# Performance work log

Measured on AMD Instinct MI355X. Metric: run time of the kernel, lower is better.

## Reference

```python
import jax, jax.numpy as jnp
import numpy as np

N, E, G = 50000, 800000, 512
C = 128          # in_channels = hidden_out_channel = out_channel
K = 3            # Chebyshev order (nb_filters)
NUM_EMB = 119    # largest OGB atom feature cardinality (padded common table)
EPS = 1e-5


def setup_inputs() -> dict:
    key = jax.random.key(0)
    ks = jax.random.split(key, 12)
    s = 0.05
    return {
        "atom_emb": jax.random.normal(ks[0], (9, NUM_EMB, C), jnp.float32) * s,
        "W1": jax.random.normal(ks[1], (K, C, C), jnp.float32) * s,
        "b1": jnp.zeros((C,), jnp.float32),
        "W3": jax.random.normal(ks[2], (K, C, C), jnp.float32) * s,
        "b3": jnp.zeros((C,), jnp.float32),
        "gamma": jnp.ones((C,), jnp.float32),
        "beta": jnp.zeros((C,), jnp.float32),
        "lw1": jax.random.normal(ks[3], (C, 16), jnp.float32) * s,
        "lb1": jnp.zeros((16,), jnp.float32),
        "lw2": jax.random.normal(ks[4], (16, 2), jnp.float32) * s,
        "lb2": jnp.zeros((2,), jnp.float32),
        "x": jax.random.randint(ks[5], (N, 9), 0, 2),
        "edge_index": jax.random.randint(ks[6], (2, E), 0, N),
        "batch": jnp.sort(jax.random.randint(ks[7], (N,), 0, G)),
    }


def _cheb_conv(h, row, col, norm, W, b):
    # PyG ChebConv, sym norm, lambda_max=2 => Lhat = -D^{-1/2} A D^{-1/2} (zero diag)
    def Lhat(z):
        return jax.ops.segment_sum(norm[:, None] * z[col], row, num_segments=N)
    Tx1 = Lhat(h)                      # T_1 = Lhat x
    Tx2 = 2.0 * Lhat(Tx1) - h          # T_2 = 2 Lhat T_1 - T_0
    return h @ W[0] + Tx1 @ W[1] + Tx2 @ W[2] + b


def reference(atom_emb, W1, b1, W3, b3, gamma, beta, lw1, lb1, lw2, lb2,
              x, edge_index, batch):
    row, col = edge_index[0], edge_index[1]
    # symmetric normalization weights (deg computed on row, as in get_laplacian)
    deg = jax.ops.segment_sum(jnp.ones((E,), jnp.float32), row, num_segments=N)
    dis = jnp.where(deg > 0, jax.lax.rsqrt(jnp.maximum(deg, 1.0)), 0.0)
    norm = -(dis[row] * dis[col])      # [E]

    # AtomEncoder: sum of 9 per-feature embeddings -> [N, C]
    h = atom_emb[jnp.arange(9), x].sum(axis=1)

    h = jax.nn.relu(_cheb_conv(h, row, col, norm, W1, b1))   # conv1
    h = jax.nn.relu(_cheb_conv(h, row, col, norm, W3, b3))   # conv3 (conv2 unused)

    # BatchNorm over nodes (training-mode batch stats, biased var)
    mu = h.mean(axis=0)
    var = jnp.mean((h - mu) ** 2, axis=0)
    h = (h - mu) * jax.lax.rsqrt(var + EPS) * gamma + beta

    # global_mean_pool over graphs
    sums = jax.ops.segment_sum(h, batch, num_segments=G)
    cnt = jax.ops.segment_sum(jnp.ones((N,), jnp.float32), batch, num_segments=G)
    pooled = sums / jnp.maximum(cnt, 1.0)[:, None]           # [G, C]

    out = jax.nn.relu(pooled @ lw1 + lb1) @ lw2 + lb2        # [G, 2]
    return out
```

## Files before the change

### kernel.cpp

```cpp
#include <hip/hip_runtime.h>
#include <hip/hip_bf16.h>

typedef __hip_bfloat16 bf16;
#define BN_EPS 1e-5f

typedef __attribute__((ext_vector_type(8))) short bf16x8;
typedef __attribute__((ext_vector_type(4))) float f32x4;

__device__ __forceinline__ float b2f(bf16 v){ return __bfloat162float(v); }
__device__ __forceinline__ float bu2f(unsigned short u){
  union { unsigned int i; float f; } x; x.i = ((unsigned int)u) << 16; return x.f;
}
__device__ __forceinline__ unsigned short f2bu(float f){
  bf16 b = __float2bfloat16(f);
  union { bf16 b; unsigned short u; } x; x.b = b; return x.u;
}
__device__ __forceinline__ float ldw(const void* p, size_t i, int wf){
  return wf ? ((const float*)p)[i] : b2f(((const bf16*)p)[i]);
}
__device__ __forceinline__ void up2(unsigned int w, float& lo, float& hi){
  union { unsigned int i; float f; } L, H;
  L.i = w << 16; H.i = w & 0xffff0000u;
  lo = L.f; hi = H.f;
}

__global__ void k_zero(int* __restrict__ p, int n,
                       const unsigned int* __restrict__ gbits, int* __restrict__ flag){
  int i = blockIdx.x * blockDim.x + threadIdx.x;
  if (i == 0) *flag = (gbits[0] == 0x3F800000u) ? 1 : 0;
  if (i < n) p[i] = 0;
}

__global__ __launch_bounds__(256) void k_bhist(const int* __restrict__ row, int E,
                                               int* __restrict__ gcnt){
  __shared__ int hist[256];
  int t = threadIdx.x;
  hist[t] = 0;
  __syncthreads();
  int base = blockIdx.x * 4096;
  #pragma unroll
  for (int j = 0; j < 16; ++j){
    int e = base + (j << 8) + t;
    if (e < E) atomicAdd(&hist[row[e] >> 8], 1);
  }
  __syncthreads();
  int h = hist[t];
  if (h > 0) atomicAdd(&gcnt[t], h);
}

__global__ __launch_bounds__(256) void k_bbase(const int* __restrict__ gcnt,
    int* __restrict__ bucketBase, int* __restrict__ gcur, int* __restrict__ rp, int N){
  __shared__ int ss[256];
  int t = threadIdx.x;
  int v = gcnt[t];
  ss[t] = v; __syncthreads();
  for (int o = 1; o < 256; o <<= 1){
    int u = (t >= o) ? ss[t - o] : 0;
    __syncthreads();
    ss[t] += u;
    __syncthreads();
  }
  int ex = ss[t] - v;
  bucketBase[t] = ex;
  gcur[t] = ex;
  if (t == 255){ bucketBase[256] = ss[255]; rp[N] = ss[255]; }
}

__global__ __launch_bounds__(256) void k_prep(int N,
    const void* __restrict__ Wa, unsigned short* __restrict__ WTa,
    const void* __restrict__ Wb, unsigned short* __restrict__ WTb,
    const void* __restrict__ emb, const int* __restrict__ x, int NE,
    unsigned short* __restrict__ h, const int* __restrict__ flag){
  int b = blockIdx.x;
  int t = threadIdx.x;
  int wf = *flag;
  if (b < 384){
    int id = b * 256 + t;
    const void* W = (id < 49152) ? Wa : Wb;
    unsigned short* WT = (id < 49152) ? WTa : WTb;
    int i = (id < 49152) ? id : id - 49152;
    int r = i >> 7, n = i & 127;
    WT[(size_t)n * 384 + r] = f2bu(ldw(W, (size_t)r * 128 + n, wf));
    return;
  }
  int gid = (b - 384) * 256 + t;
  int n = gid >> 4, c8 = (gid & 15) << 3;
  if (n >= N) return;
  float s[8];
  #pragma unroll
  for (int j = 0; j < 8; ++j) s[j] = 0.f;
  #pragma unroll
  for (int f = 0; f < 9; ++f){
    int idx = x[n * 9 + f];
    size_t base = ((size_t)(f * NE + idx) << 7) + c8;
    if (wf){
      const float* ep = (const float*)emb + base;
      #pragma unroll
      for (int j = 0; j < 8; ++j) s[j] += ep[j];
    } else {
      uint4 v = *(const uint4*)((const unsigned short*)emb + base);
      float lo, hi;
      up2(v.x, lo, hi); s[0] += lo; s[1] += hi;
      up2(v.y, lo, hi); s[2] += lo; s[3] += hi;
      up2(v.z, lo, hi); s[4] += lo; s[5] += hi;
      up2(v.w, lo, hi); s[6] += lo; s[7] += hi;
    }
  }
  uint4 r;
  r.x = ((unsigned int)f2bu(s[1]) << 16) | f2bu(s[0]);
  r.y = ((unsigned int)f2bu(s[3]) << 16) | f2bu(s[2]);
  r.z = ((unsigned int)f2bu(s[5]) << 16) | f2bu(s[4]);
  r.w = ((unsigned int)f2bu(s[7]) << 16) | f2bu(s[6]);
  *(uint4*)(h + ((size_t)n << 7) + c8) = r;
}

__global__ __launch_bounds__(256) void k_bfill1(const int* __restrict__ row,
    const int* __restrict__ col, int E,
    int* __restrict__ gcur, unsigned int* __restrict__ ebuf){
  __shared__ int hist[256];
  __shared__ int curs[256];
  int t = threadIdx.x;
  hist[t] = 0;
  __syncthreads();
  int base = blockIdx.x * 4096;
  int r[16], c[16];
  #pragma unroll
  for (int j = 0; j < 16; ++j){
    int e = base + (j << 8) + t;
    if (e < E){
      r[j] = row[e]; c[j] = col[e];
      atomicAdd(&hist[r[j] >> 8], 1);
    } else r[j] = -1;
  }
  __syncthreads();
  int h = hist[t];
  if (h > 0) curs[t] = atomicAdd(&gcur[t], h);
  __syncthreads();
  #pragma unroll
  for (int j = 0; j < 16; ++j){
    if (r[j] >= 0){
      int p = atomicAdd(&curs[r[j] >> 8], 1);
      ebuf[p] = ((unsigned int)c[j] << 8) | ((unsigned int)r[j] & 255u);
    }
  }
}

__global__ __launch_bounds__(256) void k_bfill2a(const unsigned int* __restrict__ ebuf,
    const int* __restrict__ bucketBase, int N,
    int* __restrict__ rp, float* __restrict__ dis){
  __shared__ int cnt[256];
  __shared__ int ss[256];
  int b = blockIdx.x, t = threadIdx.x;
  cnt[t] = 0;
  __syncthreads();
  int beg = bucketBase[b], end = bucketBase[b + 1];
  for (int p = beg + t; p < end; p += 256)
    atomicAdd(&cnt[ebuf[p] & 255u], 1);
  __syncthreads();
  int v = cnt[t];
  ss[t] = v; __syncthreads();
  for (int o = 1; o < 256; o <<= 1){
    int u = (t >= o) ? ss[t - o] : 0;
    __syncthreads();
    ss[t] += u;
    __syncthreads();
  }
  int idx = (b << 8) + t;
  if (idx < N){
    rp[idx] = beg + ss[t] - v;
    dis[idx] = (v > 0) ? rsqrtf((float)v) : 0.f;
  }
}

__global__ __launch_bounds__(256) void k_bfill2b(const unsigned int* __restrict__ ebuf,
    const int* __restrict__ bucketBase, const int* __restrict__ rp, int N,
    const float* __restrict__ dis, int2* __restrict__ cpack){
  __shared__ int lcur[256];
  __shared__ float sdis[256];
  int b = blockIdx.x, t = threadIdx.x;
  int idx = (b << 8) + t;
  lcur[t] = (idx < N) ? rp[idx] : 0;
  sdis[t] = (idx < N) ? dis[idx] : 0.f;
  __syncthreads();
  int beg = bucketBase[b], end = bucketBase[b + 1];
  for (int p = beg + t; p < end; p += 256){
    unsigned int pw = ebuf[p];
    int c = (int)(pw >> 8);
    int rl = (int)(pw & 255u);
    float nm = -(sdis[rl] * dis[c]);
    int slot = atomicAdd(&lcur[rl], 1);
    cpack[slot] = make_int2(c, __float_as_int(nm));
  }
}

__global__ __launch_bounds__(256) void k_spmm(const unsigned short* __restrict__ in,
    const int* __restrict__ rp, const int2* __restrict__ cpack,
    float alpha, const unsigned short* __restrict__ other, float beta,
    unsigned short* __restrict__ out, int N){
  int w = (blockIdx.x * 256 + threadIdx.x) >> 6;
  int lane = threadIdx.x & 63;
  if (w >= N) return;
  int half = lane >> 5, hl = lane & 31;
  int p0 = rp[w], p1 = rp[w + 1];
  float a0 = 0.f, a1 = 0.f, a2 = 0.f, a3 = 0.f;
  for (int p = p0; p < p1; p += 64){
    int m = p1 - p; if (m > 64) m = 64;
    int cj = 0; float nj = 0.f;
    if (lane < m){
      int2 pk = cpack[p + lane];
      cj = pk.x; nj = __int_as_float(pk.y);
    }
    for (int j = 0; j < m; j += 4){
      int e0 = j + half, e1 = j + 2 + half;
      int c0 = (e0 < m) ? __shfl(cj, e0) : -1;
      float w0 = __shfl(nj, e0);
      int c1 = (e1 < m) ? __shfl(cj, e1) : -1;
      float w1 = __shfl(nj, e1);
      if (c0 >= 0){
        ushort4 v = *(const ushort4*)(in + (((size_t)c0) << 7) + (hl << 2));
        a0 += w0 * bu2f(v.x); a1 += w0 * bu2f(v.y);
        a2 += w0 * bu2f(v.z); a3 += w0 * bu2f(v.w);
      }
      if (c1 >= 0){
        ushort4 v = *(const ushort4*)(in + (((size_t)c1) << 7) + (hl << 2));
        a0 += w1 * bu2f(v.x); a1 += w1 * bu2f(v.y);
        a2 += w1 * bu2f(v.z); a3 += w1 * bu2f(v.w);
      }
    }
  }
  a0 += __shfl_xor(a0, 32);
  a1 += __shfl_xor(a1, 32);
  a2 += __shfl_xor(a2, 32);
  a3 += __shfl_xor(a3, 32);
  if (half == 0){
    size_t o = (((size_t)w) << 7) + (hl << 2);
    a0 *= alpha; a1 *= alpha; a2 *= alpha; a3 *= alpha;
    if (other){
      ushort4 ov = *(const ushort4*)(other + o);
      a0 += beta * bu2f(ov.x); a1 += beta * bu2f(ov.y);
      a2 += beta * bu2f(ov.z); a3 += beta * bu2f(ov.w);
    }
    ushort4 r;
    r.x = f2bu(a0); r.y = f2bu(a1); r.z = f2bu(a2); r.w = f2bu(a3);
    *(ushort4*)(out + o) = r;
  }
}

__global__ __launch_bounds__(256) void k_conv(const unsigned short* __restrict__ X,
    const unsigned short* __restrict__ T1, const unsigned short* __restrict__ T2,
    const unsigned short* __restrict__ WT,
    const void* __restrict__ bias,
    unsigned short* __restrict__ Y, int N, const int* __restrict__ flag,
    float* __restrict__ bns){
  int wf = *flag;
  __shared__ unsigned short As[128 * 40];
  __shared__ unsigned short Ws[128 * 40];
  int t = threadIdx.x;
  int wv = t >> 6, lane = t & 63;
  int m16 = lane & 15, quad = lane >> 4;
  int n0 = blockIdx.x * 128;

  f32x4 acc[2][8];
  #pragma unroll
  for (int i = 0; i < 2; ++i)
    #pragma unroll
    for (int j = 0; j < 8; ++j) acc[i][j] = (f32x4){0.f, 0.f, 0.f, 0.f};

  for (int kc = 0; kc < 12; ++kc){
    const unsigned short* src = (kc < 4) ? X : ((kc < 8) ? T1 : T2);
    int koff = (kc & 3) << 5;
    int kg = kc << 5;
    #pragma unroll
    for (int i = 0; i < 2; ++i){
      int id = t + (i << 8);
      int r = id >> 2, ks = id & 3;
      int node = n0 + r;
      uint4 v = make_uint4(0, 0, 0, 0);
      if (node < N) v = *(const uint4*)(src + ((size_t)node << 7) + koff + (ks << 3));
      *(uint4*)((void*)(As + r * 40 + (ks << 3))) = v;
    }
    #pragma unroll
    for (int i = 0; i < 2; ++i){
      int id = t + (i << 8);
      int n = id >> 2, ks = id & 3;
      uint4 v = *(const uint4*)(WT + (size_t)n * 384 + kg + (ks << 3));
      *(uint4*)((void*)(Ws + n * 40 + (ks << 3))) = v;
    }
    __syncthreads();
    bf16x8 af[2];
    af[0] = *(const bf16x8*)((const void*)(As + (32 * wv + m16) * 40 + (quad << 3)));
    af[1] = *(const bf16x8*)((const void*)(As + (32 * wv + 16 + m16) * 40 + (quad << 3)));
    #pragma unroll
    for (int tn = 0; tn < 8; ++tn){
      bf16x8 bf_ = *(const bf16x8*)((const void*)(Ws + (16 * tn + m16) * 40 + (quad << 3)));
      acc[0][tn] = __builtin_amdgcn_mfma_f32_16x16x32_bf16(af[0], bf_, acc[0][tn], 0, 0, 0);
      acc[1][tn] = __builtin_amdgcn_mfma_f32_16x16x32_bf16(af[1], bf_, acc[1][tn], 0, 0, 0);
    }
    __syncthreads();
  }
  float bv[8];
  #pragma unroll
  for (int tn = 0; tn < 8; ++tn) bv[tn] = ldw(bias, 16 * tn + m16, wf);
  float ps[8], pq[8];
  #pragma unroll
  for (int tn = 0; tn < 8; ++tn){ ps[tn] = 0.f; pq[tn] = 0.f; }
  #pragma unroll
  for (int ri = 0; ri < 2; ++ri){
    #pragma unroll
    for (int r = 0; r < 4; ++r){
      int node = n0 + 32 * wv + 16 * ri + quad * 4 + r;
      if (node < N){
        #pragma unroll
        for (int tn = 0; tn < 8; ++tn){
          float v = fmaxf(acc[ri][tn][r] + bv[tn], 0.f);
          Y[((size_t)node << 7) + 16 * tn + m16] = f2bu(v);
          ps[tn] += v; pq[tn] += v * v;
        }
      }
    }
  }
  if (bns){
    float* redf = (float*)As;
    int rg = (wv << 2) | quad;
    #pragma unroll
    for (int tn = 0; tn < 8; ++tn) redf[rg * 128 + tn * 16 + m16] = ps[tn];
    __syncthreads();
    if (t < 128){
      float a = 0.f;
      #pragma unroll
      for (int r = 0; r < 16; ++r) a += redf[r * 128 + t];
      atomicAdd(&bns[t], a);
    }
    __syncthreads();
    #pragma unroll
    for (int tn = 0; tn < 8; ++tn) redf[rg * 128 + tn * 16 + m16] = pq[tn];
    __syncthreads();
    if (t < 128){
      float a = 0.f;
      #pragma unroll
      for (int r = 0; r < 16; ++r) a += redf[r * 128 + t];
      atomicAdd(&bns[128 + t], a);
    }
  }
}

__device__ __forceinline__ int lbound(const int* a, int n, int key){
  int lo = 0, hi = n;
  while (lo < hi){ int mid = (lo + hi) >> 1; if (a[mid] < key) lo = mid + 1; else hi = mid; }
  return lo;
}

__global__ __launch_bounds__(128) void k_pool(const unsigned short* __restrict__ h,
    const int* __restrict__ batchv, int N, const float* __restrict__ bns,
    const void* __restrict__ gamma, const void* __restrict__ beta,
    const void* __restrict__ lw1, const void* __restrict__ lb1,
    const void* __restrict__ lw2, const void* __restrict__ lb2,
    void* __restrict__ out, const int* __restrict__ flag){
  int wf = *flag;
  int g = blockIdx.x;
  int t = threadIdx.x;
  int c8 = (t & 15) << 3;
  int rg = t >> 4;
  __shared__ int slo, shi;
  if (t == 0){ slo = lbound(batchv, N, g); shi = lbound(batchv, N, g + 1); }
  __syncthreads();
  int lo = slo, hi = shi, cnt = hi - lo;
  float s[8];
  #pragma unroll
  for (int j = 0; j < 8; ++j) s[j] = 0.f;
  for (int n = lo + rg; n < hi; n += 8){
    uint4 v = *(const uint4*)(h + ((size_t)n << 7) + c8);
    float a, b;
    up2(v.x, a, b); s[0] += a; s[1] += b;
    up2(v.y, a, b); s[2] += a; s[3] += b;
    up2(v.z, a, b); s[4] += a; s[5] += b;
    up2(v.w, a, b); s[6] += a; s[7] += b;
  }
  __shared__ float red[8][128];
  *(float4*)(&red[rg][c8])     = (float4){s[0], s[1], s[2], s[3]};
  *(float4*)(&red[rg][c8 + 4]) = (float4){s[4], s[5], s[6], s[7]};
  __syncthreads();
  int c = t;
  float acc = 0.f;
  #pragma unroll
  for (int r = 0; r < 8; ++r) acc += red[r][c];
  float pooled = acc / (float)(cnt > 0 ? cnt : 1);
  float mu = bns[c] / (float)N;
  float var = bns[128 + c] / (float)N - mu * mu;
  float sc = ldw(gamma, c, wf) * rsqrtf(var + BN_EPS);
  float sh = ldw(beta, c, wf) - mu * sc;
  float pb = (cnt > 0) ? (pooled * sc + sh) : 0.f;
  __shared__ float sp[128];
  __shared__ float hid[16];
  sp[c] = pb; __syncthreads();
  if (c < 16){
    float sm = ldw(lb1, c, wf);
    for (int i = 0; i < 128; ++i) sm += sp[i] * ldw(lw1, i * 16 + c, wf);
    hid[c] = fmaxf(sm, 0.f);
  }
  __syncthreads();
  if (c < 2){
    float sm = ldw(lb2, c, wf);
    for (int j = 0; j < 16; ++j) sm += hid[j] * ldw(lw2, j * 2 + c, wf);
    if (wf) ((float*)out)[g * 2 + c] = sm;
    else    ((bf16*)out)[g * 2 + c] = __float2bfloat16(sm);
  }
}

extern "C" void kernel_launch(void* const* d_in, const int* in_sizes, int n_in,
                              void* d_out, int out_size, void* d_ws, size_t ws_size,
                              hipStream_t stream){
  const void* emb   = d_in[0];
  const void* W1    = d_in[1];
  const void* b1    = d_in[2];
  const void* W3    = d_in[3];
  const void* b3    = d_in[4];
  const void* gamma = d_in[5];
  const void* beta  = d_in[6];
  const void* lw1   = d_in[7];
  const void* lb1   = d_in[8];
  const void* lw2   = d_in[9];
  const void* lb2   = d_in[10];
  const int* x      = (const int*)d_in[11];
  const int* ei     = (const int*)d_in[12];
  const int* batchv = (const int*)d_in[13];
  (void)n_in; (void)ws_size;

  int N  = in_sizes[13];
  int E  = in_sizes[12] / 2;
  int NE = in_sizes[0] / (9 * 128);
  int G  = out_size / 2;
  const int* row = ei;
  const int* col = ei + E;

  char* ws = (char*)d_ws;
  size_t off = 0;
  auto alloc = [&](size_t bytes) -> char* {
    char* p = ws + off;
    off += (bytes + 255) & ~(size_t)255;
    return p;
  };
  int*   flag = (int*)alloc(4);
  int*   gcnt = (int*)alloc(256 * 4);
  float* bns  = (float*)alloc(256 * 4);
  int*   bucketBase = (int*)alloc(257 * 4);
  int*   gcur = (int*)alloc(256 * 4);
  int*   rp   = (int*)alloc((size_t)(N + 1) * 4);
  float* dis  = (float*)alloc((size_t)N * 4);
  unsigned int* ebuf = (unsigned int*)alloc((size_t)E * 4);
  int2*  cpack = (int2*)alloc((size_t)E * 8);
  unsigned short* wt1 = (unsigned short*)alloc(49152 * 2);
  unsigned short* wt2 = (unsigned short*)alloc(49152 * 2);
  size_t fb = ((size_t)N * 128 * 2 + 255) & ~(size_t)255;
  unsigned short* Hf = (unsigned short*)alloc(fb);
  unsigned short* Tf = (unsigned short*)alloc(fb);
  unsigned short* Zf = (unsigned short*)alloc(fb);

  k_zero<<<2, 256, 0, stream>>>(gcnt, 512, (const unsigned int*)gamma, flag);

  int ebk = (E + 4095) / 4096;
  int NB  = (N + 255) / 256;
  k_bhist<<<ebk, 256, 0, stream>>>(row, E, gcnt);
  k_bbase<<<1, 256, 0, stream>>>(gcnt, bucketBase, gcur, rp, N);
  int pb = 384 + (int)(((size_t)N * 16 + 255) / 256);
  k_prep<<<pb, 256, 0, stream>>>(N, W1, wt1, W3, wt2, emb, x, NE, Hf, flag);
  k_bfill1<<<ebk, 256, 0, stream>>>(row, col, E, gcur, ebuf);
  k_bfill2a<<<NB, 256, 0, stream>>>(ebuf, bucketBase, N, rp, dis);
  k_bfill2b<<<NB, 256, 0, stream>>>(ebuf, bucketBase, rp, N, dis, cpack);

  int sb = (N + 3) / 4;
  int cb = (N + 127) / 128;
  k_spmm<<<sb, 256, 0, stream>>>(Hf, rp, cpack, 1.f, nullptr, 0.f, Tf, N);
  k_spmm<<<sb, 256, 0, stream>>>(Tf, rp, cpack, 2.f, Hf, -1.f, Zf, N);
  k_conv<<<cb, 256, 0, stream>>>(Hf, Tf, Zf, wt1, b1, Hf, N, flag, nullptr);
  k_spmm<<<sb, 256, 0, stream>>>(Hf, rp, cpack, 1.f, nullptr, 0.f, Tf, N);
  k_spmm<<<sb, 256, 0, stream>>>(Tf, rp, cpack, 2.f, Hf, -1.f, Zf, N);
  k_conv<<<cb, 256, 0, stream>>>(Hf, Tf, Zf, wt2, b3, Hf, N, flag, bns);

  k_pool<<<G, 128, 0, stream>>>(Hf, batchv, N, bns, gamma, beta, lw1, lb1, lw2, lb2,
                                d_out, flag);
}
```

Before: 352.6 us.

## Fold Chebyshev T2 recurrence into weights and widen SpMM gather to 16-byte loads

Uses the identity T2 = 2·L·T1 − X to fold the recurrence into the weight matrices at prep time: W0' = W0 − W2 and W2' = 2·W2. The SpMM kernel then writes the raw L·T1 result without the axpy epilogue. The SpMM is also restructured so that four quarter-waves each process different edges with 8-channel uint4 loads, then reduce across quarters with shuffles. This removes the extra read of the 'other' tensor and the cross-lane broadcast of edge data. The cost is a slight change to bf16 rounding behaviour.

```diff
diff --git a/kernel.cpp b/kernel.cpp
--- a/kernel.cpp
+++ b/kernel.cpp
@@ -80,7 +80,12 @@
     unsigned short* WT = (id < 49152) ? WTa : WTb;
     int i = (id < 49152) ? id : id - 49152;
     int r = i >> 7, n = i & 127;
-    WT[(size_t)n * 384 + r] = f2bu(ldw(W, (size_t)r * 128 + n, wf));
+    float v;
+    if (r < 128)       v = ldw(W, (size_t)r * 128 + n, wf)
+                         - ldw(W, ((size_t)(256 + r)) * 128 + n, wf);
+    else if (r < 256)  v = ldw(W, (size_t)r * 128 + n, wf);
+    else               v = 2.f * ldw(W, (size_t)r * 128 + n, wf);
+    WT[(size_t)n * 384 + r] = f2bu(v);
     return;
   }
   int gid = (b - 384) * 256 + t;
@@ -195,54 +200,58 @@
 
 __global__ __launch_bounds__(256) void k_spmm(const unsigned short* __restrict__ in,
     const int* __restrict__ rp, const int2* __restrict__ cpack,
-    float alpha, const unsigned short* __restrict__ other, float beta,
     unsigned short* __restrict__ out, int N){
   int w = (blockIdx.x * 256 + threadIdx.x) >> 6;
+  if (w >= N) return;
   int lane = threadIdx.x & 63;
-  if (w >= N) return;
-  int half = lane >> 5, hl = lane & 31;
-  int p0 = rp[w], p1 = rp[w + 1];
+  int quad = lane >> 4, ql = lane & 15;
+  int p1 = rp[w + 1];
+  int p = rp[w] + quad;
+  const unsigned short* inq = in + (ql << 3);
   float a0 = 0.f, a1 = 0.f, a2 = 0.f, a3 = 0.f;
-  for (int p = p0; p < p1; p += 64){
-    int m = p1 - p; if (m > 64) m = 64;
-    int cj = 0; float nj = 0.f;
-    if (lane < m){
-      int2 pk = cpack[p + lane];
-      cj = pk.x; nj = __int_as_float(pk.y);
-    }
-    for (int j = 0; j < m; j += 4){
-      int e0 = j + half, e1 = j + 2 + half;
-      int c0 = (e0 < m) ? __shfl(cj, e0) : -1;
-      float w0 = __shfl(nj, e0);
-      int c1 = (e1 < m) ? __shfl(cj, e1) : -1;
-      float w1 = __shfl(nj, e1);
-      if (c0 >= 0){
-        ushort4 v = *(const ushort4*)(in + (((size_t)c0) << 7) + (hl << 2));
-        a0 += w0 * bu2f(v.x); a1 += w0 * bu2f(v.y);
-        a2 += w0 * bu2f(v.z); a3 += w0 * bu2f(v.w);
-      }
-      if (c1 >= 0){
-        ushort4 v = *(const ushort4*)(in + (((size_t)c1) << 7) + (hl << 2));
-        a0 += w1 * bu2f(v.x); a1 += w1 * bu2f(v.y);
-        a2 += w1 * bu2f(v.z); a3 += w1 * bu2f(v.w);
-      }
-    }
-  }
-  a0 += __shfl_xor(a0, 32);
-  a1 += __shfl_xor(a1, 32);
-  a2 += __shfl_xor(a2, 32);
-  a3 += __shfl_xor(a3, 32);
-  if (half == 0){
-    size_t o = (((size_t)w) << 7) + (hl << 2);
-    a0 *= alpha; a1 *= alpha; a2 *= alpha; a3 *= alpha;
-    if (other){
-      ushort4 ov = *(const ushort4*)(other + o);
-      a0 += beta * bu2f(ov.x); a1 += beta * bu2f(ov.y);
-      a2 += beta * bu2f(ov.z); a3 += beta * bu2f(ov.w);
-    }
-    ushort4 r;
-    r.x = f2bu(a0); r.y = f2bu(a1); r.z = f2bu(a2); r.w = f2bu(a3);
-    *(ushort4*)(out + o) = r;
+  float a4 = 0.f, a5 = 0.f, a6 = 0.f, a7 = 0.f;
+  for (; p + 4 < p1; p += 8){
+    int2 e0 = cpack[p];
+    int2 e1 = cpack[p + 4];
+    uint4 v0 = *(const uint4*)(inq + ((size_t)e0.x << 7));
+    uint4 v1 = *(const uint4*)(inq + ((size_t)e1.x << 7));
+    float w0 = __int_as_float(e0.y);
+    float w1 = __int_as_float(e1.y);
+    float lo, hi;
+    up2(v0.x, lo, hi); a0 += w0 * lo; a1 += w0 * hi;
+    up2(v0.y, lo, hi); a2 += w0 * lo; a3 += w0 * hi;
+    up2(v0.z, lo, hi); a4 += w0 * lo; a5 += w0 * hi;
+    up2(v0.w, lo, hi); a6 += w0 * lo; a7 += w0 * hi;
+    up2(v1.x, lo, hi); a0 += w1 * lo; a1 += w1 * hi;
+    up2(v1.y, lo, hi); a2 += w1 * lo; a3 += w1 * hi;
+    up2(v1.z, lo, hi); a4 += w1 * lo; a5 += w1 * hi;
+    up2(v1.w, lo, hi); a6 += w1 * lo; a7 += w1 * hi;
+  }
+  if (p < p1){
+    int2 e0 = cpack[p];
+    uint4 v0 = *(const uint4*)(inq + ((size_t)e0.x << 7));
+    float w0 = __int_as_float(e0.y);
+    float lo, hi;
+    up2(v0.x, lo, hi); a0 += w0 * lo; a1 += w0 * hi;
+    up2(v0.y, lo, hi); a2 += w0 * lo; a3 += w0 * hi;
+    up2(v0.z, lo, hi); a4 += w0 * lo; a5 += w0 * hi;
+    up2(v0.w, lo, hi); a6 += w0 * lo; a7 += w0 * hi;
+  }
+  a0 += __shfl_xor(a0, 16); a0 += __shfl_xor(a0, 32);
+  a1 += __shfl_xor(a1, 16); a1 += __shfl_xor(a1, 32);
+  a2 += __shfl_xor(a2, 16); a2 += __shfl_xor(a2, 32);
+  a3 += __shfl_xor(a3, 16); a3 += __shfl_xor(a3, 32);
+  a4 += __shfl_xor(a4, 16); a4 += __shfl_xor(a4, 32);
+  a5 += __shfl_xor(a5, 16); a5 += __shfl_xor(a5, 32);
+  a6 += __shfl_xor(a6, 16); a6 += __shfl_xor(a6, 32);
+  a7 += __shfl_xor(a7, 16); a7 += __shfl_xor(a7, 32);
+  if (quad == 0){
+    uint4 r;
+    r.x = ((unsigned int)f2bu(a1) << 16) | f2bu(a0);
+    r.y = ((unsigned int)f2bu(a3) << 16) | f2bu(a2);
+    r.z = ((unsigned int)f2bu(a5) << 16) | f2bu(a4);
+    r.w = ((unsigned int)f2bu(a7) << 16) | f2bu(a6);
+    *(uint4*)(out + ((size_t)w << 7) + (ql << 3)) = r;
   }
 }
 
@@ -470,11 +479,11 @@
 
   int sb = (N + 3) / 4;
   int cb = (N + 127) / 128;
-  k_spmm<<<sb, 256, 0, stream>>>(Hf, rp, cpack, 1.f, nullptr, 0.f, Tf, N);
-  k_spmm<<<sb, 256, 0, stream>>>(Tf, rp, cpack, 2.f, Hf, -1.f, Zf, N);
+  k_spmm<<<sb, 256, 0, stream>>>(Hf, rp, cpack, Tf, N);
+  k_spmm<<<sb, 256, 0, stream>>>(Tf, rp, cpack, Zf, N);
   k_conv<<<cb, 256, 0, stream>>>(Hf, Tf, Zf, wt1, b1, Hf, N, flag, nullptr);
-  k_spmm<<<sb, 256, 0, stream>>>(Hf, rp, cpack, 1.f, nullptr, 0.f, Tf, N);
-  k_spmm<<<sb, 256, 0, stream>>>(Tf, rp, cpack, 2.f, Hf, -1.f, Zf, N);
+  k_spmm<<<sb, 256, 0, stream>>>(Hf, rp, cpack, Tf, N);
+  k_spmm<<<sb, 256, 0, stream>>>(Tf, rp, cpack, Zf, N);
   k_conv<<<cb, 256, 0, stream>>>(Hf, Tf, Zf, wt2, b3, Hf, N, flag, bns);
 
   k_pool<<<G, 128, 0, stream>>>(Hf, batchv, N, bns, gamma, beta, lw1, lb1, lw2, lb2,
```

New measurement: 320.2 us. 1.1x faster.
